# Optimization experiments

Measured on AMD Instinct MI355X. Metric: run time of the kernel, lower is better.

## Reference

```python
import jax, jax.numpy as jnp
import numpy as np

N = 262144       # batch rows
C = 256          # in_channels
K = 256          # uint8 code range


def setup_inputs() -> dict:
    key = jax.random.key(0)
    k1, k2, k3, k4 = jax.random.split(key, 4)
    left = jax.random.randint(k1, (N, C), 0, K, dtype=jnp.int32)
    right = jax.random.randint(k2, (N, C), 0, K, dtype=jnp.int32)
    # per-channel 256x256 lookup tables: white_table[c][l, r] -> new code in [0, 256)
    white_table = jax.random.randint(k3, (C, K, K), 0, K, dtype=jnp.int32)
    # per-channel last-layer codebook: last_codebook[c][1][code] -> float
    codebook = jax.random.normal(k4, (C, K), dtype=jnp.float32)
    return {"left": left, "right": right, "white_table": white_table, "codebook": codebook}


def reference(left, right, white_table, codebook):
    # Fused equivalent of the per-channel python loop:
    #   for c: codes[:, c] = white_table[c][left[:, c], right[:, c]]
    #   out[:, c]  = codebook[c][codes[:, c]]
    ch = jnp.arange(C, dtype=jnp.int32)[None, :]          # [1, C] broadcasts vs [N, C]
    codes = white_table[ch, left, right]                   # [N, C] int32 gather
    out = codebook[ch, codes]                              # [N, C] float32 gather
    return out
```

## Files before the change

### kernel.cpp

```cpp
#include <hip/hip_runtime.h>
#include <stdint.h>

#define CCH 256
#define KK  256

typedef int   i32x4 __attribute__((ext_vector_type(4)));
typedef float f32x4 __attribute__((ext_vector_type(4)));
typedef unsigned short u16x4 __attribute__((ext_vector_type(4)));
typedef unsigned short u16x8 __attribute__((ext_vector_type(8)));

__global__ __launch_bounds__(256) void compress_table_kernel(
    const int4* __restrict__ t, uchar4* __restrict__ o, int n4) {
  int i = blockIdx.x * 256 + threadIdx.x;
  if (i < n4) {
    int4 v = t[i];
    o[i] = make_uchar4((unsigned char)v.x, (unsigned char)v.y,
                       (unsigned char)v.z, (unsigned char)v.w);
  }
}

__global__ __launch_bounds__(256, 3) void transpose_pack_kernel(
    const i32x4* __restrict__ L4, const i32x4* __restrict__ R4,
    unsigned short* __restrict__ LRtT, int n0_base, int nslice) {
  __shared__ unsigned short tile[32 * 260];
  const int T     = 8;
  const int tile0 = blockIdx.x * T;
  const int tid   = threadIdx.x;
  const int w     = tid >> 6;
  const int lq    = tid & 63;

  i32x4 Lb[8], Rb[8];
  {
    const size_t rowbase = (size_t)(n0_base + tile0 * 32);
#pragma unroll
    for (int p = 0; p < 8; ++p) {
      const size_t gi = (rowbase + p * 4 + w) * 64 + lq;
      Lb[p] = L4[gi];
      Rb[p] = R4[gi];
    }
  }

#pragma unroll 1
  for (int t = 0; t < T; ++t) {
#pragma unroll
    for (int p = 0; p < 8; ++p) {
      u16x4 pk;
      pk[0] = (unsigned short)((Lb[p][0] << 8) | Rb[p][0]);
      pk[1] = (unsigned short)((Lb[p][1] << 8) | Rb[p][1]);
      pk[2] = (unsigned short)((Lb[p][2] << 8) | Rb[p][2]);
      pk[3] = (unsigned short)((Lb[p][3] << 8) | Rb[p][3]);
      *(u16x4*)&tile[(p * 4 + w) * 260 + lq * 4] = pk;
    }
    if (t + 1 < T) {
      const size_t rowbase = (size_t)(n0_base + (tile0 + t + 1) * 32);
#pragma unroll
      for (int p = 0; p < 8; ++p) {
        const size_t gi = (rowbase + p * 4 + w) * 64 + lq;
        Lb[p] = L4[gi];
        Rb[p] = R4[gi];
      }
    }
    asm volatile("s_waitcnt lgkmcnt(0)" ::: "memory");
    __builtin_amdgcn_s_barrier();

    {
      unsigned short col[32];
#pragma unroll
      for (int r = 0; r < 32; ++r) col[r] = tile[r * 260 + tid];
      u16x8 s0, s1, s2, s3;
#pragma unroll
      for (int j = 0; j < 8; ++j) {
        s0[j] = col[j];
        s1[j] = col[8 + j];
        s2[j] = col[16 + j];
        s3[j] = col[24 + j];
      }
      unsigned short* dst = LRtT + ((size_t)(tile0 + t) * CCH + tid) * 32;
      *(u16x8*)(dst + 0)  = s0;
      *(u16x8*)(dst + 8)  = s1;
      *(u16x8*)(dst + 16) = s2;
      *(u16x8*)(dst + 24) = s3;
    }
    asm volatile("s_waitcnt lgkmcnt(0)" ::: "memory");
    __builtin_amdgcn_s_barrier();
  }
}

__global__ __launch_bounds__(512, 4) void code_gather_kernel(
    const unsigned short* __restrict__ LRtT, const unsigned char* __restrict__ tab8,
    unsigned char* __restrict__ codes, int nslice) {
  __shared__ unsigned char tabs[KK * KK];
  const int c   = blockIdx.x & (CCH - 1);
  const int sub = blockIdx.x >> 8;
  const int tid = threadIdx.x;
  const int tbase = sub * 1024;

  u16x8 v[8];
#pragma unroll
  for (int i = 0; i < 8; ++i) {
    const size_t a =
        ((size_t)(tbase + i * 128 + (tid >> 2)) * CCH + c) * 32 + (tid & 3) * 8;
    v[i] = *(const u16x8*)(LRtT + a);
  }
  {
    const int4* src = (const int4*)(tab8 + (size_t)c * (KK * KK));
    int4* dst = (int4*)tabs;
#pragma unroll
    for (int i = 0; i < 8; ++i) dst[i * 512 + tid] = src[i * 512 + tid];
  }
  __syncthreads();

  uint2* outp = (uint2*)(codes + (size_t)c * nslice + (size_t)sub * 32768);
#pragma unroll
  for (int i = 0; i < 8; ++i) {
    unsigned lo = (unsigned)tabs[v[i][0]] | ((unsigned)tabs[v[i][1]] << 8) |
                  ((unsigned)tabs[v[i][2]] << 16) | ((unsigned)tabs[v[i][3]] << 24);
    unsigned hi = (unsigned)tabs[v[i][4]] | ((unsigned)tabs[v[i][5]] << 8) |
                  ((unsigned)tabs[v[i][6]] << 16) | ((unsigned)tabs[v[i][7]] << 24);
    outp[i * 512 + tid] = make_uint2(lo, hi);
  }
}

__global__ __launch_bounds__(512, 6) void codebook_transpose_kernel(
    const unsigned char* __restrict__ codes, const float* __restrict__ cb,
    float* __restrict__ out, int n0_base, int nslice) {
  __shared__ float    cbs[32 * KK];
  __shared__ unsigned ctd[32 * 65];
  const int cg = blockIdx.x & 7;
  const int tn = blockIdx.x >> 3;
  const int c0 = cg * 32;
  const int tid = threadIdx.x;

  {
    const f32x4* cbg = (const f32x4*)(cb + (size_t)c0 * KK);
    f32x4* cbl = (f32x4*)cbs;
#pragma unroll
    for (int i = 0; i < 4; ++i) cbl[i * 512 + tid] = cbg[i * 512 + tid];
  }
  {
    const int cc = tid >> 4;
    const int s  = tid & 15;
    const uint4 val = *(const uint4*)(codes + (size_t)(c0 + cc) * nslice +
                                      (size_t)tn * 256 + s * 16);
    const int d0 = cc * 65 + s * 4;
    ctd[d0 + 0] = val.x;
    ctd[d0 + 1] = val.y;
    ctd[d0 + 2] = val.z;
    ctd[d0 + 3] = val.w;
  }
  __syncthreads();

  const int cq = tid & 7;
  const int nb = tid >> 3;
  const unsigned cw0 = ctd[(cq * 4 + 0) * 65 + nb];
  const unsigned cw1 = ctd[(cq * 4 + 1) * 65 + nb];
  const unsigned cw2 = ctd[(cq * 4 + 2) * 65 + nb];
  const unsigned cw3 = ctd[(cq * 4 + 3) * 65 + nb];
  const float* b0 = cbs + (cq * 4 + 0) * KK;
  const float* b1 = cbs + (cq * 4 + 1) * KK;
  const float* b2 = cbs + (cq * 4 + 2) * KK;
  const float* b3 = cbs + (cq * 4 + 3) * KK;
  float* ob = out + (size_t)(n0_base + tn * 256 + nb * 4) * CCH + c0 + cq * 4;
#pragma unroll
  for (int k = 0; k < 4; ++k) {
    f32x4 o;
    o[0] = b0[(cw0 >> (8 * k)) & 255u];
    o[1] = b1[(cw1 >> (8 * k)) & 255u];
    o[2] = b2[(cw2 >> (8 * k)) & 255u];
    o[3] = b3[(cw3 >> (8 * k)) & 255u];
    __builtin_nontemporal_store(o, (f32x4*)(ob + (size_t)k * CCH));
  }
}

#define ROWS_PER_BLOCK 512
#define NGROUPS 16
#define GCH (CCH / NGROUPS)

template <typename TabT>
__global__ __launch_bounds__(256, 8) void gather_kernel(
    const i32x4* __restrict__ left, const i32x4* __restrict__ right,
    const TabT* __restrict__ tab, const float* __restrict__ cb,
    f32x4* __restrict__ out, int nrows) {
  __shared__ float cbs[GCH * KK];
  const int g     = blockIdx.x & (NGROUPS - 1);
  const int chunk = blockIdx.x / NGROUPS;
  const int q     = threadIdx.x & 3;
  const int rsub  = threadIdx.x >> 2;
  {
    const f32x4* cbg = (const f32x4*)(cb + (size_t)(g * GCH) * KK);
    f32x4* cbl = (f32x4*)cbs;
#pragma unroll
    for (int i = 0; i < 4; ++i) cbl[threadIdx.x + i * 256] = cbg[threadIdx.x + i * 256];
  }
  __syncthreads();
  const int cbase  = g * GCH + q * 4;
  const TabT* t0   = tab + (size_t)cbase * (KK * KK);
  const int vecoff = g * 4 + q;
  const float* cq  = cbs + (q * 4) * KK;
  const int rbase = chunk * ROWS_PER_BLOCK;
#pragma unroll
  for (int it = 0; it < ROWS_PER_BLOCK / 32; ++it) {
    const int r0 = rbase + it * 32 + rsub;
    if (r0 >= nrows) break;
    const unsigned v0 = (unsigned)r0 * 64u + (unsigned)vecoff;
    i32x4 L0 = left[v0];
    i32x4 R0 = right[v0];
    unsigned c0 = (unsigned)t0[          (unsigned)(L0[0] * KK + R0[0])];
    unsigned c1 = (unsigned)t0[ 65536u + (unsigned)(L0[1] * KK + R0[1])];
    unsigned c2 = (unsigned)t0[131072u + (unsigned)(L0[2] * KK + R0[2])];
    unsigned c3 = (unsigned)t0[196608u + (unsigned)(L0[3] * KK + R0[3])];
    f32x4 o;
    o[0] = cq[       c0];
    o[1] = cq[KK   + c1];
    o[2] = cq[2*KK + c2];
    o[3] = cq[3*KK + c3];
    out[v0] = o;
  }
}

extern "C" void kernel_launch(void* const* d_in, const int* in_sizes, int n_in,
                              void* d_out, int out_size, void* d_ws, size_t ws_size,
                              hipStream_t stream) {
  const int*   left  = (const int*)d_in[0];
  const int*   right = (const int*)d_in[1];
  const int*   wt    = (const int*)d_in[2];
  const float* cb    = (const float*)d_in[3];
  float* out = (float*)d_out;

  const int nrows = in_sizes[0] / CCH;
  const int tab_elems = CCH * KK * KK;
  const size_t tab_bytes = (size_t)tab_elems;

  int S = 0;
  for (int s = 1; s <= 8; s <<= 1) {
    if (nrows % (s * 32768)) continue;
    size_t need = tab_bytes + (size_t)768 * (size_t)(nrows / s);
    if (need <= ws_size) { S = s; break; }
  }

  if (S) {
    unsigned char* tab8 = (unsigned char*)d_ws;
    int n4 = tab_elems / 4;
    compress_table_kernel<<<n4 / 256, 256, 0, stream>>>(
        (const int4*)wt, (uchar4*)tab8, n4);

    const int nslice = nrows / S;
    unsigned short* LRtT = (unsigned short*)((char*)d_ws + tab_bytes);
    unsigned char* codes = (unsigned char*)d_ws + tab_bytes + (size_t)512 * nslice;

    for (int h = 0; h < S; ++h) {
      const int n0 = h * nslice;
      transpose_pack_kernel<<<nslice / 256, 256, 0, stream>>>(
          (const i32x4*)left, (const i32x4*)right, LRtT, n0, nslice);
      code_gather_kernel<<<(nslice / 32768) * CCH, 512, 0, stream>>>(
          LRtT, tab8, codes, nslice);
      codebook_transpose_kernel<<<(nslice / 256) * 8, 512, 0, stream>>>(
          codes, cb, out, n0, nslice);
    }
  } else if (ws_size >= tab_bytes) {
    unsigned char* tab8 = (unsigned char*)d_ws;
    int n4 = tab_elems / 4;
    compress_table_kernel<<<n4 / 256, 256, 0, stream>>>(
        (const int4*)wt, (uchar4*)tab8, n4);
    const int blocks = ((nrows + ROWS_PER_BLOCK - 1) / ROWS_PER_BLOCK) * NGROUPS;
    gather_kernel<unsigned char><<<blocks, 256, 0, stream>>>(
        (const i32x4*)left, (const i32x4*)right, tab8, cb, (f32x4*)out, nrows);
  } else {
    const int blocks = ((nrows + ROWS_PER_BLOCK - 1) / ROWS_PER_BLOCK) * NGROUPS;
    gather_kernel<int><<<blocks, 256, 0, stream>>>(
        (const i32x4*)left, (const i32x4*)right, wt, cb, (f32x4*)out, nrows);
  }
}
```

Baseline: 728.5 us.

## Use direct global-to-LDS loads with double buffering in transpose and table staging

The transpose_pack kernel is rewritten so that 512-thread blocks use global_load_lds to stream L and R rows straight into a double-buffered LDS area. One step's loads overlap the previous step's pack-and-transpose, and the pack now reads columns directly from LDS rather than going through registers and a staging tile. The code_gather kernel's 64KB per-channel table copy into LDS also switches to global_load_lds, skipping the register round trip. The cost is hand-tuned vmcnt waits and lower occupancy (64KB of LDS per block, launch bounds of one block), and the whole scheme depends on the global_load_lds builtin's ordering behaving as assumed.

Result: slower. 753.4 us (+3.4%).

```diff
diff --git a/kernel.cpp b/kernel.cpp
--- a/kernel.cpp
+++ b/kernel.cpp
@@ -6,8 +6,13 @@
 
 typedef int   i32x4 __attribute__((ext_vector_type(4)));
 typedef float f32x4 __attribute__((ext_vector_type(4)));
-typedef unsigned short u16x4 __attribute__((ext_vector_type(4)));
 typedef unsigned short u16x8 __attribute__((ext_vector_type(8)));
+
+typedef const __attribute__((address_space(1))) void gas_t;
+typedef __attribute__((address_space(3))) void las_t;
+__device__ __forceinline__ void gl_lds16(const void* g, void* l) {
+  __builtin_amdgcn_global_load_lds((gas_t*)g, (las_t*)l, 16, 0, 0);
+}
 
 __global__ __launch_bounds__(256) void compress_table_kernel(
     const int4* __restrict__ t, uchar4* __restrict__ o, int n4) {
@@ -19,71 +24,65 @@
   }
 }
 
-__global__ __launch_bounds__(256, 3) void transpose_pack_kernel(
-    const i32x4* __restrict__ L4, const i32x4* __restrict__ R4,
+__global__ __launch_bounds__(512, 1) void transpose_pack_kernel(
+    const unsigned char* __restrict__ Lg, const unsigned char* __restrict__ Rg,
     unsigned short* __restrict__ LRtT, int n0_base, int nslice) {
-  __shared__ unsigned short tile[32 * 260];
-  const int T     = 8;
-  const int tile0 = blockIdx.x * T;
-  const int tid   = threadIdx.x;
-  const int w     = tid >> 6;
-  const int lq    = tid & 63;
-
-  i32x4 Lb[8], Rb[8];
-  {
-    const size_t rowbase = (size_t)(n0_base + tile0 * 32);
-#pragma unroll
-    for (int p = 0; p < 8; ++p) {
-      const size_t gi = (rowbase + p * 4 + w) * 64 + lq;
-      Lb[p] = L4[gi];
-      Rb[p] = R4[gi];
-    }
-  }
-
+  __shared__ unsigned int lds[2][8192];
+  const int tid  = threadIdx.x;
+  const int w    = tid >> 6;
+  const int lane = tid & 63;
+  const int g0   = blockIdx.x * 16;
+  const bool isR = (w >= 4);
+  const int  wi  = w & 3;
+  const unsigned char* src = isR ? Rg : Lg;
+  const int ldsoff = (isR ? 4096 : 0) + wi * 4 * 256;
+
+  const int c  = tid >> 1;
+  const int hh = tid & 1;
+
+#define ISSUE(t, b)                                                            \
+  {                                                                            \
+    const unsigned char* p = src +                                             \
+        ((size_t)(n0_base + (g0 + (t)) * 16) + (size_t)(wi * 4)) * 1024 +      \
+        lane * 16;                                                             \
+    unsigned int* d = &lds[b][ldsoff];                                         \
+    gl_lds16(p,        d);                                                     \
+    gl_lds16(p + 1024, d + 256);                                               \
+    gl_lds16(p + 2048, d + 512);                                               \
+    gl_lds16(p + 3072, d + 768);                                               \
+  }
+
+#define PHASE_B(t, b)                                                          \
+  {                                                                            \
+    const unsigned int* Lr = &lds[b][0];                                       \
+    const unsigned int* Rr = &lds[b][4096];                                    \
+    u16x8 v;                                                                   \
+    _Pragma("unroll")                                                          \
+    for (int r = 0; r < 8; ++r) {                                              \
+      unsigned lv = Lr[(hh * 8 + r) * 256 + c];                                \
+      unsigned rv = Rr[(hh * 8 + r) * 256 + c];                                \
+      v[r] = (unsigned short)((lv << 8) | rv);                                 \
+    }                                                                          \
+    const int gt = g0 + (t);                                                   \
+    *(u16x8*)&LRtT[((size_t)(gt >> 1) * 256 + c) * 32 + (gt & 1) * 16 +        \
+                   hh * 8] = v;                                                \
+  }
+
+  ISSUE(0, 0);
 #pragma unroll 1
-  for (int t = 0; t < T; ++t) {
-#pragma unroll
-    for (int p = 0; p < 8; ++p) {
-      u16x4 pk;
-      pk[0] = (unsigned short)((Lb[p][0] << 8) | Rb[p][0]);
-      pk[1] = (unsigned short)((Lb[p][1] << 8) | Rb[p][1]);
-      pk[2] = (unsigned short)((Lb[p][2] << 8) | Rb[p][2]);
-      pk[3] = (unsigned short)((Lb[p][3] << 8) | Rb[p][3]);
-      *(u16x4*)&tile[(p * 4 + w) * 260 + lq * 4] = pk;
-    }
-    if (t + 1 < T) {
-      const size_t rowbase = (size_t)(n0_base + (tile0 + t + 1) * 32);
-#pragma unroll
-      for (int p = 0; p < 8; ++p) {
-        const size_t gi = (rowbase + p * 4 + w) * 64 + lq;
-        Lb[p] = L4[gi];
-        Rb[p] = R4[gi];
-      }
-    }
-    asm volatile("s_waitcnt lgkmcnt(0)" ::: "memory");
+  for (int t = 0; t < 15; ++t) {
+    ISSUE(t + 1, (t + 1) & 1);
+    if (t == 0) asm volatile("s_waitcnt vmcnt(4)" ::: "memory");
+    else        asm volatile("s_waitcnt vmcnt(5)" ::: "memory");
     __builtin_amdgcn_s_barrier();
-
-    {
-      unsigned short col[32];
-#pragma unroll
-      for (int r = 0; r < 32; ++r) col[r] = tile[r * 260 + tid];
-      u16x8 s0, s1, s2, s3;
-#pragma unroll
-      for (int j = 0; j < 8; ++j) {
-        s0[j] = col[j];
-        s1[j] = col[8 + j];
-        s2[j] = col[16 + j];
-        s3[j] = col[24 + j];
-      }
-      unsigned short* dst = LRtT + ((size_t)(tile0 + t) * CCH + tid) * 32;
-      *(u16x8*)(dst + 0)  = s0;
-      *(u16x8*)(dst + 8)  = s1;
-      *(u16x8*)(dst + 16) = s2;
-      *(u16x8*)(dst + 24) = s3;
-    }
-    asm volatile("s_waitcnt lgkmcnt(0)" ::: "memory");
+    PHASE_B(t, t & 1);
     __builtin_amdgcn_s_barrier();
   }
+  asm volatile("s_waitcnt vmcnt(1)" ::: "memory");
+  __builtin_amdgcn_s_barrier();
+  PHASE_B(15, 1);
+#undef ISSUE
+#undef PHASE_B
 }
 
 __global__ __launch_bounds__(512, 4) void code_gather_kernel(
@@ -103,10 +102,11 @@
     v[i] = *(const u16x8*)(LRtT + a);
   }
   {
-    const int4* src = (const int4*)(tab8 + (size_t)c * (KK * KK));
-    int4* dst = (int4*)tabs;
-#pragma unroll
-    for (int i = 0; i < 8; ++i) dst[i * 512 + tid] = src[i * 512 + tid];
+    const int w = tid >> 6, lane = tid & 63;
+    const unsigned char* tsrc = tab8 + (size_t)c * (KK * KK) + w * 8192 + lane * 16;
+    unsigned int* tdst = (unsigned int*)tabs + w * 2048;
+#pragma unroll
+    for (int i = 0; i < 8; ++i) gl_lds16(tsrc + i * 1024, tdst + i * 256);
   }
   __syncthreads();
 
@@ -250,8 +250,9 @@
 
     for (int h = 0; h < S; ++h) {
       const int n0 = h * nslice;
-      transpose_pack_kernel<<<nslice / 256, 256, 0, stream>>>(
-          (const i32x4*)left, (const i32x4*)right, LRtT, n0, nslice);
+      transpose_pack_kernel<<<nslice / 256, 512, 0, stream>>>(
+          (const unsigned char*)left, (const unsigned char*)right, LRtT, n0,
+          nslice);
       code_gather_kernel<<<(nslice / 32768) * CCH, 512, 0, stream>>>(
           LRtT, tab8, codes, nslice);
       codebook_transpose_kernel<<<(nslice / 256) * 8, 512, 0, stream>>>(
```
